# Kernel tuning notes

Measured on AMD Instinct MI355X. Metric: run time of the kernel, lower is better.

The kernel has to match this reference:

```python
import jax, jax.numpy as jnp
import numpy as np

F = 64          # n_features
H = F * F       # n_hidden = 4096
P = 4           # proj_size
T = 8192        # timesteps


def _proj_lstm_cell_zero_state(x, W_ih, W_hh, b_ih, b_hh, W_hr):
    """One PyTorch proj-LSTM layer applied per-timestep with zero initial
    (h, c). x: [T, in_dim] -> [T, P].  With h0=0, W_hh contributes 0 and
    f*c_prev vanishes."""
    h0 = jnp.zeros((x.shape[0], W_hh.shape[1]), x.dtype)
    gates = x @ W_ih.T + h0 @ W_hh.T + b_ih + b_hh          # [T, 4H]
    i, f, g, o = jnp.split(gates, 4, axis=-1)               # PyTorch gate order
    c = jax.nn.sigmoid(i) * jnp.tanh(g)                     # f*c0 = 0
    h = jax.nn.sigmoid(o) * jnp.tanh(c)                     # [T, H]
    return h @ W_hr.T                                       # [T, P]


def setup_inputs() -> dict:
    key = jax.random.key(0)
    ks = jax.random.split(key, 17)
    s = 0.05
    d = {"x": jax.random.normal(ks[0], (T, F), jnp.float32)}
    shapes = {
        "W_ih_0": (4 * H, F), "W_hh_0": (4 * H, P), "b_ih_0": (4 * H,),
        "b_hh_0": (4 * H,), "W_hr_0": (P, H),
        "W_ih_1": (4 * H, P), "W_hh_1": (4 * H, P), "b_ih_1": (4 * H,),
        "b_hh_1": (4 * H,), "W_hr_1": (P, H),
        "W_ih_2": (4 * H, P), "W_hh_2": (4 * H, P), "b_ih_2": (4 * H,),
        "b_hh_2": (4 * H,), "W_hr_2": (P, H),
    }
    for i, (name, shp) in enumerate(shapes.items()):
        d[name] = s * jax.random.normal(ks[i + 1], shp, jnp.float32)
    return d


def reference(x,
              W_ih_0, W_hh_0, b_ih_0, b_hh_0, W_hr_0,
              W_ih_1, W_hh_1, b_ih_1, b_hh_1, W_hr_1,
              W_ih_2, W_hh_2, b_ih_2, b_hh_2, W_hr_2):
    # study(): inputs.split(1, dim=0) feeds each timestep as a fresh length-1
    # sequence with zero initial state, so timesteps are independent ->
    # vectorize over T instead of the per-step Python loop.
    h = _proj_lstm_cell_zero_state(x, W_ih_0, W_hh_0, b_ih_0, b_hh_0, W_hr_0)
    h = _proj_lstm_cell_zero_state(h, W_ih_1, W_hh_1, b_ih_1, b_hh_1, W_hr_1)
    h = _proj_lstm_cell_zero_state(h, W_ih_2, W_hh_2, b_ih_2, b_hh_2, W_hr_2)
    return h  # [T, P]
```

## Files before the change

### kernel.cpp

```cpp
#include <hip/hip_runtime.h>

#define TSTEPS 8192
#define HDIM 4096
#define PDIM 4
#define KDIM 64

typedef unsigned short u16;
typedef __attribute__((ext_vector_type(8))) short short8;
typedef __attribute__((ext_vector_type(4))) float f32x4;

#define S1 -1.44269504089f
#define S2 -2.88539008177f

#if __has_builtin(__builtin_amdgcn_exp2f)
#define EXP2(x) __builtin_amdgcn_exp2f(x)
#else
#define EXP2(x) exp2f(x)
#endif
__device__ __forceinline__ float rcpf(float x) { return __builtin_amdgcn_rcpf(x); }

__device__ __forceinline__ float h_merge(float c, float ec) {
  float c2 = c * c;
  float num = c * fmaf(c2, 10.0f, 105.0f);
  float den = fmaf(c2, 45.0f, 105.0f) + c2 * c2;
  return num * rcpf(den * (1.0f + ec));
}

__device__ __forceinline__ float sig_poly(float z) {
  float z2 = z * z;
  float q = fmaf(z2, -2.1081349e-4f, 2.0833333e-3f);
  q = fmaf(z2, q, -2.0833333e-2f);
  q = fmaf(z2, q, 0.25f);
  return fmaf(z, q, 0.5f);
}
__device__ __forceinline__ float tanh_poly(float z) {
  float z2 = z * z;
  float q = fmaf(z2, -5.3968254e-2f, 1.3333333e-1f);
  q = fmaf(z2, q, -3.3333333e-1f);
  q = fmaf(z2, q, 1.0f);
  return z * q;
}

__device__ __forceinline__ void gload16(const void* g, void* l) {
  __builtin_amdgcn_global_load_lds((const __attribute__((address_space(1))) unsigned int*)g,
                                   (__attribute__((address_space(3))) unsigned int*)l,
                                   16, 0, 0);
}

__device__ __forceinline__ u16 bf16_rne(float f) {
  unsigned u = __float_as_uint(f);
  u += 0x7FFF + ((u >> 16) & 1);
  return (u16)(u >> 16);
}
__device__ __forceinline__ void hilo(float v, u16& h, u16& l) {
  h = bf16_rne(v);
  l = bf16_rne(v - __uint_as_float((unsigned)h << 16));
}

#define WS_Y0   0
#define WS_Y1   32768
#define WS_BSC  65536
#define WS_C1   77824
#define WS_C2   159744
#define WS_XHI  241664
#define WS_XLO  503808
#define WS_WHI  765952
#define WS_WLO  1159168
#define WS_PP   1552384

__global__ void prep_kernel(const float* __restrict__ x,
                            const float* __restrict__ Wih0, const float* __restrict__ bih0,
                            const float* __restrict__ bhh0,
                            const float* __restrict__ Wih1, const float* __restrict__ bih1,
                            const float* __restrict__ bhh1, const float* __restrict__ Whr1,
                            const float* __restrict__ Wih2, const float* __restrict__ bih2,
                            const float* __restrict__ bhh2, const float* __restrict__ Whr2,
                            float* __restrict__ ws) {
  const int i = blockIdx.x * 256 + threadIdx.x;
  u16* xhi = (u16*)(ws + WS_XHI);
  u16* xlo = (u16*)(ws + WS_XLO);
  u16* whi = (u16*)(ws + WS_WHI);
  u16* wlo = (u16*)(ws + WS_WLO);

  if (i < 131072) {
    float4 v = *(const float4*)&x[i * 4];
    float val[4] = {v.x, v.y, v.z, v.w};
    u16 h[4], l[4];
#pragma unroll
    for (int e = 0; e < 4; ++e) hilo(val[e], h[e], l[e]);
    *(ushort4*)&xhi[i * 4] = make_ushort4(h[0], h[1], h[2], h[3]);
    *(ushort4*)&xlo[i * 4] = make_ushort4(l[0], l[1], l[2], l[3]);
  } else if (i < 327680) {
    int f = i - 131072;
    int el4 = f * 4;
    int r = el4 >> 6;
    int k4 = el4 & 63;
    int gate = r >> 12, jr = r & 4095;
    int src = (gate == 0) ? jr : (gate + 1) * HDIM + jr;
    float sc = (gate == 1) ? S2 : S1;
    float4 v = *(const float4*)&Wih0[(size_t)src * KDIM + k4];
    float val[4] = {sc * v.x, sc * v.y, sc * v.z, sc * v.w};
    u16 h[4], l[4];
#pragma unroll
    for (int e = 0; e < 4; ++e) hilo(val[e], h[e], l[e]);
    *(ushort4*)&whi[r * KDIM + k4] = make_ushort4(h[0], h[1], h[2], h[3]);
    *(ushort4*)&wlo[r * KDIM + k4] = make_ushort4(l[0], l[1], l[2], l[3]);
  } else if (i < 339968) {
    int f = i - 327680;
    int g = f >> 12, j = f & 4095;
    int src = (g == 0) ? j : (g + 1) * HDIM + j;
    float sc = (g == 1) ? S2 : S1;
    ws[WS_BSC + f] = sc * (bih0[src] + bhh0[src]);
  } else if (i < 348160) {
    int f = i - 339968;
    const float* Wih = (f < 4096) ? Wih1 : Wih2;
    const float* bih = (f < 4096) ? bih1 : bih2;
    const float* bhh = (f < 4096) ? bhh1 : bhh2;
    const float* Whr = (f < 4096) ? Whr1 : Whr2;
    float* c = ws + ((f < 4096) ? WS_C1 : WS_C2);
    int j = f & 4095;
    float4 wi = *(const float4*)&Wih[(size_t)j * 4];
    float4 wg = *(const float4*)&Wih[(size_t)(2 * HDIM + j) * 4];
    float4 wo = *(const float4*)&Wih[(size_t)(3 * HDIM + j) * 4];
    float* cb = c + j * 20;
    *(float4*)(cb + 0)  = wi;
    *(float4*)(cb + 4)  = wg;
    *(float4*)(cb + 8)  = wo;
    *(float4*)(cb + 12) = make_float4(bih[j] + bhh[j],
                                      bih[2 * HDIM + j] + bhh[2 * HDIM + j],
                                      bih[3 * HDIM + j] + bhh[3 * HDIM + j], 0.f);
    *(float4*)(cb + 16) = make_float4(Whr[j], Whr[HDIM + j], Whr[2 * HDIM + j], Whr[3 * HDIM + j]);
  }
}

__global__ __launch_bounds__(256, 2)
void lstm_layer0_mfma(const u16* __restrict__ xhi, const u16* __restrict__ xlo,
                      const u16* __restrict__ whi, const u16* __restrict__ wlo,
                      const float* __restrict__ bsc, const float* __restrict__ Whr,
                      float* __restrict__ pp) {
  __shared__ __align__(16) char smem[65536];
  u16* lw_hi = (u16*)smem;
  u16* lw_lo = (u16*)(smem + 24576);
  u16* lx    = (u16*)(smem + 49152);

  const int tid = threadIdx.x;
  const int w = tid >> 6, lane = tid & 63;
  const int m = lane & 15, q = lane >> 4;
  const int jb = blockIdx.x & 63, tbb = blockIdx.x >> 6;
  const int j0 = jb * 64;
  const int t0 = tbb * 256;

  const int r8_ = lane >> 3;
  const int swo = ((lane & 7) ^ r8_) * 8;

#pragma unroll
  for (int ui = 0; ui < 16; ++ui) {
    const int u = w * 16 + ui;
    const u16* g;
    char* l;
    if (u < 24) {
      g = whi + (size_t)((u >> 3) * HDIM + j0 + (u & 7) * 8 + r8_) * 64 + swo;
      l = smem + u * 1024;
    } else if (u < 48) {
      int uu = u - 24;
      g = wlo + (size_t)((uu >> 3) * HDIM + j0 + (uu & 7) * 8 + r8_) * 64 + swo;
      l = smem + 24576 + uu * 1024;
    } else {
      int uu = u - 48;
      g = xhi + (size_t)(t0 + uu * 8 + r8_) * 64 + swo;
      l = smem + 49152 + uu * 1024;
    }
    gload16(g, l);
  }

  float whr_v[4][4];
#pragma unroll
  for (int p = 0; p < 4; ++p)
#pragma unroll
    for (int js = 0; js < 4; ++js)
      whr_v[p][js] = Whr[(size_t)p * HDIM + j0 + js * 16 + m];
  float biv[4], bgv[4], bov[4];
#pragma unroll
  for (int js = 0; js < 4; ++js) {
    const int j = j0 + js * 16 + m;
    biv[js] = bsc[j];
    bgv[js] = bsc[HDIM + j];
    bov[js] = bsc[2 * HDIM + j];
  }

  f32x4 acc[2][4][3];
  short8 al[2][2];

  auto zero_acc = [&]() {
#pragma unroll
    for (int ts = 0; ts < 2; ++ts)
#pragma unroll
      for (int js = 0; js < 4; ++js)
#pragma unroll
        for (int g = 0; g < 3; ++g) acc[ts][js][g] = (f32x4){0.f, 0.f, 0.f, 0.f};
  };
  auto load_al = [&](int tt) {
#pragma unroll
    for (int kc = 0; kc < 2; ++kc)
#pragma unroll
      for (int ts = 0; ts < 2; ++ts)
        al[kc][ts] = *(const short8*)&xlo[(size_t)(t0 + tt * 128 + w * 32 + ts * 16 + m) * KDIM + kc * 32 + q * 8];
  };
  auto compute = [&]() {
#pragma unroll
    for (int kc = 0; kc < 2; ++kc) {
      const int cs = ((kc * 4 + q) ^ (m & 7)) * 8;
      short8 ah[2];
#pragma unroll
      for (int ts = 0; ts < 2; ++ts)
        ah[ts] = *(const short8*)&lx[(w * 32 + ts * 16 + m) * 64 + cs];
#pragma unroll
      for (int js = 0; js < 4; ++js) {
#pragma unroll
        for (int g = 0; g < 3; ++g) {
          const int roff = (g * 64 + js * 16 + m) * 64 + cs;
          short8 bh = *(const short8*)&lw_hi[roff];
          short8 bl = *(const short8*)&lw_lo[roff];
#pragma unroll
          for (int ts = 0; ts < 2; ++ts) {
            acc[ts][js][g] = __builtin_amdgcn_mfma_f32_16x16x32_bf16(ah[ts], bh, acc[ts][js][g], 0, 0, 0);
            acc[ts][js][g] = __builtin_amdgcn_mfma_f32_16x16x32_bf16(al[kc][ts], bh, acc[ts][js][g], 0, 0, 0);
            acc[ts][js][g] = __builtin_amdgcn_mfma_f32_16x16x32_bf16(ah[ts], bl, acc[ts][js][g], 0, 0, 0);
          }
        }
      }
    }
  };
  auto act_proj = [&](int tt) {
    float hreg[2][4][4];
#pragma unroll
    for (int js = 0; js < 4; ++js) {
#pragma unroll
      for (int ts = 0; ts < 2; ++ts) {
#pragma unroll
        for (int r = 0; r < 4; ++r) {
          float ea = EXP2(acc[ts][js][0][r] + biv[js]);
          float eb = EXP2(acc[ts][js][1][r] + bgv[js]);
          float c = (1.0f - eb) * rcpf((1.0f + ea) * (1.0f + eb));
          float ec = EXP2(acc[ts][js][2][r] + bov[js]);
          hreg[ts][js][r] = h_merge(c, ec);
        }
      }
    }
#pragma unroll
    for (int ts = 0; ts < 2; ++ts) {
#pragma unroll
      for (int r = 0; r < 4; ++r) {
        float pv[4];
#pragma unroll
        for (int p = 0; p < 4; ++p) {
          float s = 0.f;
#pragma unroll
          for (int js = 0; js < 4; ++js) s = fmaf(hreg[ts][js][r], whr_v[p][js], s);
#pragma unroll
          for (int ofs = 1; ofs < 16; ofs <<= 1) s += __shfl_xor(s, ofs, 16);
          pv[p] = s;
        }
        if (m == 0) {
          const int t = t0 + tt * 128 + w * 32 + ts * 16 + q * 4 + r;
          *(float4*)&pp[((size_t)jb * TSTEPS + t) * PDIM] = make_float4(pv[0], pv[1], pv[2], pv[3]);
        }
      }
    }
  };

  load_al(0);
  zero_acc();
  __syncthreads();
  compute();
  __syncthreads();
#pragma unroll
  for (int ui = 0; ui < 4; ++ui) {
    const int u = w * 4 + ui;
    gload16(xhi + (size_t)(t0 + 128 + u * 8 + r8_) * 64 + swo, smem + 49152 + u * 1024);
  }
  load_al(1);
  act_proj(0);
  zero_acc();
  __syncthreads();
  compute();
  act_proj(1);
}

__global__ void reduce64(const float* __restrict__ pp, float* __restrict__ y) {
  const int i = blockIdx.x * 256 + threadIdx.x;
  float s = 0.f;
#pragma unroll 16
  for (int k = 0; k < 64; ++k) s += pp[(size_t)k * (TSTEPS * PDIM) + i];
  y[i] = s;
}

__global__ __launch_bounds__(256, 4)
void lstm_small(const float* __restrict__ xin, const float* __restrict__ cpk,
                float* __restrict__ pp) {
  __shared__ __align__(16) float rec[1280];
  const int tid = threadIdx.x;
  const int tc = blockIdx.x >> 6;
  const int jsp = blockIdx.x & 63;
  const int j0 = jsp * 64;

  for (int i = tid; i < 320; i += 256)
    ((float4*)rec)[i] = ((const float4*)(cpk + (size_t)j0 * 20))[i];

  const int tbase = tc * 1024 + tid;
  float4 xv[4];
#pragma unroll
  for (int s = 0; s < 4; ++s) xv[s] = ((const float4*)xin)[tbase + s * 256];
  float o[4][4];
#pragma unroll
  for (int s = 0; s < 4; ++s)
#pragma unroll
    for (int p = 0; p < 4; ++p) o[s][p] = 0.f;
  __syncthreads();

#pragma unroll 2
  for (int jj = 0; jj < 64; ++jj) {
    const float* cb = rec + jj * 20;
    float4 wi = *(const float4*)(cb + 0);
    float4 wg = *(const float4*)(cb + 4);
    float4 wo = *(const float4*)(cb + 8);
    float4 bb = *(const float4*)(cb + 12);
    float4 wr = *(const float4*)(cb + 16);
#pragma unroll
    for (int s = 0; s < 4; ++s) {
      float gi = bb.x, gg = bb.y, go = bb.z;
      gi = fmaf(xv[s].x, wi.x, gi); gi = fmaf(xv[s].y, wi.y, gi);
      gi = fmaf(xv[s].z, wi.z, gi); gi = fmaf(xv[s].w, wi.w, gi);
      gg = fmaf(xv[s].x, wg.x, gg); gg = fmaf(xv[s].y, wg.y, gg);
      gg = fmaf(xv[s].z, wg.z, gg); gg = fmaf(xv[s].w, wg.w, gg);
      go = fmaf(xv[s].x, wo.x, go); go = fmaf(xv[s].y, wo.y, go);
      go = fmaf(xv[s].z, wo.z, go); go = fmaf(xv[s].w, wo.w, go);
      float c = sig_poly(gi) * tanh_poly(gg);
      float h = tanh_poly(c) * sig_poly(go);
      o[s][0] = fmaf(h, wr.x, o[s][0]); o[s][1] = fmaf(h, wr.y, o[s][1]);
      o[s][2] = fmaf(h, wr.z, o[s][2]); o[s][3] = fmaf(h, wr.w, o[s][3]);
    }
  }

#pragma unroll
  for (int s = 0; s < 4; ++s)
    ((float4*)pp)[(size_t)jsp * TSTEPS + tbase + s * 256] =
        make_float4(o[s][0], o[s][1], o[s][2], o[s][3]);
}

extern "C" void kernel_launch(void* const* d_in, const int* in_sizes, int n_in,
                              void* d_out, int out_size, void* d_ws, size_t ws_size,
                              hipStream_t stream) {
  const float* x    = (const float*)d_in[0];
  const float* Wih0 = (const float*)d_in[1];
  const float* bih0 = (const float*)d_in[3];
  const float* bhh0 = (const float*)d_in[4];
  const float* Whr0 = (const float*)d_in[5];
  const float* Wih1 = (const float*)d_in[6];
  const float* bih1 = (const float*)d_in[8];
  const float* bhh1 = (const float*)d_in[9];
  const float* Whr1 = (const float*)d_in[10];
  const float* Wih2 = (const float*)d_in[11];
  const float* bih2 = (const float*)d_in[13];
  const float* bhh2 = (const float*)d_in[14];
  const float* Whr2 = (const float*)d_in[15];
  float* out = (float*)d_out;
  float* ws = (float*)d_ws;
  float* pp = ws + WS_PP;

  prep_kernel<<<dim3(1360), dim3(256), 0, stream>>>(
      x, Wih0, bih0, bhh0, Wih1, bih1, bhh1, Whr1, Wih2, bih2, bhh2, Whr2, ws);

  lstm_layer0_mfma<<<dim3(2048), dim3(256), 0, stream>>>(
      (const u16*)(ws + WS_XHI), (const u16*)(ws + WS_XLO),
      (const u16*)(ws + WS_WHI), (const u16*)(ws + WS_WLO),
      ws + WS_BSC, Whr0, pp);
  reduce64<<<dim3(128), dim3(256), 0, stream>>>(pp, ws + WS_Y0);

  lstm_small<<<dim3(512), dim3(256), 0, stream>>>(ws + WS_Y0, ws + WS_C1, pp);
  reduce64<<<dim3(128), dim3(256), 0, stream>>>(pp, ws + WS_Y1);

  lstm_small<<<dim3(512), dim3(256), 0, stream>>>(ws + WS_Y1, ws + WS_C2, pp);
  reduce64<<<dim3(128), dim3(256), 0, stream>>>(pp, out);
}
```

Before: 230.3 us.

## Fuse partial-sum reductions and both small LSTM layers into one kernel

```diff
diff --git a/kernel.cpp b/kernel.cpp
--- a/kernel.cpp
+++ b/kernel.cpp
@@ -119,17 +119,13 @@
     const float* Whr = (f < 4096) ? Whr1 : Whr2;
     float* c = ws + ((f < 4096) ? WS_C1 : WS_C2);
     int j = f & 4095;
-    float4 wi = *(const float4*)&Wih[(size_t)j * 4];
-    float4 wg = *(const float4*)&Wih[(size_t)(2 * HDIM + j) * 4];
-    float4 wo = *(const float4*)&Wih[(size_t)(3 * HDIM + j) * 4];
-    float* cb = c + j * 20;
-    *(float4*)(cb + 0)  = wi;
-    *(float4*)(cb + 4)  = wg;
-    *(float4*)(cb + 8)  = wo;
-    *(float4*)(cb + 12) = make_float4(bih[j] + bhh[j],
+    *(float4*)(c + j * 4)         = *(const float4*)&Wih[(size_t)j * 4];
+    *(float4*)(c + 16384 + j * 4) = *(const float4*)&Wih[(size_t)(2 * HDIM + j) * 4];
+    *(float4*)(c + 32768 + j * 4) = *(const float4*)&Wih[(size_t)(3 * HDIM + j) * 4];
+    *(float4*)(c + 49152 + j * 4) = make_float4(bih[j] + bhh[j],
                                       bih[2 * HDIM + j] + bhh[2 * HDIM + j],
                                       bih[3 * HDIM + j] + bhh[3 * HDIM + j], 0.f);
-    *(float4*)(cb + 16) = make_float4(Whr[j], Whr[HDIM + j], Whr[2 * HDIM + j], Whr[3 * HDIM + j]);
+    *(float4*)(c + 65536 + j * 4) = make_float4(Whr[j], Whr[HDIM + j], Whr[2 * HDIM + j], Whr[3 * HDIM + j]);
   }
 }
 
@@ -287,65 +283,93 @@
   act_proj(1);
 }
 
-__global__ void reduce64(const float* __restrict__ pp, float* __restrict__ y) {
-  const int i = blockIdx.x * 256 + threadIdx.x;
-  float s = 0.f;
-#pragma unroll 16
-  for (int k = 0; k < 64; ++k) s += pp[(size_t)k * (TSTEPS * PDIM) + i];
-  y[i] = s;
-}
-
-__global__ __launch_bounds__(256, 4)
-void lstm_small(const float* __restrict__ xin, const float* __restrict__ cpk,
-                float* __restrict__ pp) {
-  __shared__ __align__(16) float rec[1280];
+__global__ void fused_rest(const float* __restrict__ pp,
+                           const float* __restrict__ c1, const float* __restrict__ c2,
+                           float* __restrict__ out) {
+  __shared__ float ytile[64];
+  __shared__ float part[256];
   const int tid = threadIdx.x;
-  const int tc = blockIdx.x >> 6;
-  const int jsp = blockIdx.x & 63;
-  const int j0 = jsp * 64;
-
-  for (int i = tid; i < 320; i += 256)
-    ((float4*)rec)[i] = ((const float4*)(cpk + (size_t)j0 * 20))[i];
-
-  const int tbase = tc * 1024 + tid;
-  float4 xv[4];
-#pragma unroll
-  for (int s = 0; s < 4; ++s) xv[s] = ((const float4*)xin)[tbase + s * 256];
-  float o[4][4];
-#pragma unroll
-  for (int s = 0; s < 4; ++s)
-#pragma unroll
-    for (int p = 0; p < 4; ++p) o[s][p] = 0.f;
+  const int t0 = blockIdx.x * 16;
+  const int lane = tid & 63, w = tid >> 6;
+  const int jlane = lane & 15, tg = lane >> 4;
+
+  {
+    const int o = tid & 63;
+    const int sg = tid >> 6;
+    float s = 0.f;
+#pragma unroll 4
+    for (int k = sg * 16; k < sg * 16 + 16; ++k)
+      s += pp[(size_t)k * (TSTEPS * PDIM) + t0 * PDIM + o];
+    part[sg * 64 + o] = s;
+  }
   __syncthreads();
+  if (tid < 64) ytile[tid] = part[tid] + part[64 + tid] + part[128 + tid] + part[192 + tid];
+  __syncthreads();
+
+#pragma unroll
+  for (int L = 0; L < 2; ++L) {
+    const float* c = (L == 0) ? c1 : c2;
+    const float4* cwi = (const float4*)(c);
+    const float4* cwg = (const float4*)(c + 16384);
+    const float4* cwo = (const float4*)(c + 32768);
+    const float4* cbb = (const float4*)(c + 49152);
+    const float4* cwr = (const float4*)(c + 65536);
+
+    float4 xv[4];
+#pragma unroll
+    for (int s = 0; s < 4; ++s) xv[s] = *(const float4*)&ytile[(tg * 4 + s) * 4];
+    float o_[4][4];
+#pragma unroll
+    for (int s = 0; s < 4; ++s)
+#pragma unroll
+      for (int p = 0; p < 4; ++p) o_[s][p] = 0.f;
 
 #pragma unroll 2
-  for (int jj = 0; jj < 64; ++jj) {
-    const float* cb = rec + jj * 20;
-    float4 wi = *(const float4*)(cb + 0);
-    float4 wg = *(const float4*)(cb + 4);
-    float4 wo = *(const float4*)(cb + 8);
-    float4 bb = *(const float4*)(cb + 12);
-    float4 wr = *(const float4*)(cb + 16);
-#pragma unroll
-    for (int s = 0; s < 4; ++s) {
-      float gi = bb.x, gg = bb.y, go = bb.z;
-      gi = fmaf(xv[s].x, wi.x, gi); gi = fmaf(xv[s].y, wi.y, gi);
-      gi = fmaf(xv[s].z, wi.z, gi); gi = fmaf(xv[s].w, wi.w, gi);
-      gg = fmaf(xv[s].x, wg.x, gg); gg = fmaf(xv[s].y, wg.y, gg);
-      gg = fmaf(xv[s].z, wg.z, gg); gg = fmaf(xv[s].w, wg.w, gg);
-      go = fmaf(xv[s].x, wo.x, go); go = fmaf(xv[s].y, wo.y, go);
-      go = fmaf(xv[s].z, wo.z, go); go = fmaf(xv[s].w, wo.w, go);
-      float c = sig_poly(gi) * tanh_poly(gg);
-      float h = tanh_poly(c) * sig_poly(go);
-      o[s][0] = fmaf(h, wr.x, o[s][0]); o[s][1] = fmaf(h, wr.y, o[s][1]);
-      o[s][2] = fmaf(h, wr.z, o[s][2]); o[s][3] = fmaf(h, wr.w, o[s][3]);
-    }
-  }
-
-#pragma unroll
-  for (int s = 0; s < 4; ++s)
-    ((float4*)pp)[(size_t)jsp * TSTEPS + tbase + s * 256] =
-        make_float4(o[s][0], o[s][1], o[s][2], o[s][3]);
+    for (int jj = 0; jj < 64; ++jj) {
+      const int j = w * 1024 + jj * 16 + jlane;
+      float4 wi = cwi[j];
+      float4 wg = cwg[j];
+      float4 wo = cwo[j];
+      float4 bb = cbb[j];
+      float4 wr = cwr[j];
+#pragma unroll
+      for (int s = 0; s < 4; ++s) {
+        float gi = bb.x, gg = bb.y, go = bb.z;
+        gi = fmaf(xv[s].x, wi.x, gi); gi = fmaf(xv[s].y, wi.y, gi);
+        gi = fmaf(xv[s].z, wi.z, gi); gi = fmaf(xv[s].w, wi.w, gi);
+        gg = fmaf(xv[s].x, wg.x, gg); gg = fmaf(xv[s].y, wg.y, gg);
+        gg = fmaf(xv[s].z, wg.z, gg); gg = fmaf(xv[s].w, wg.w, gg);
+        go = fmaf(xv[s].x, wo.x, go); go = fmaf(xv[s].y, wo.y, go);
+        go = fmaf(xv[s].z, wo.z, go); go = fmaf(xv[s].w, wo.w, go);
+        float cc = sig_poly(gi) * tanh_poly(gg);
+        float h = tanh_poly(cc) * sig_poly(go);
+        o_[s][0] = fmaf(h, wr.x, o_[s][0]); o_[s][1] = fmaf(h, wr.y, o_[s][1]);
+        o_[s][2] = fmaf(h, wr.z, o_[s][2]); o_[s][3] = fmaf(h, wr.w, o_[s][3]);
+      }
+    }
+
+#pragma unroll
+    for (int s = 0; s < 4; ++s)
+#pragma unroll
+      for (int p = 0; p < 4; ++p) {
+#pragma unroll
+        for (int ofs = 1; ofs < 16; ofs <<= 1)
+          o_[s][p] += __shfl_xor(o_[s][p], ofs, 16);
+      }
+    __syncthreads();
+    if (jlane == 0) {
+#pragma unroll
+      for (int s = 0; s < 4; ++s)
+#pragma unroll
+        for (int p = 0; p < 4; ++p)
+          part[w * 64 + (tg * 4 + s) * 4 + p] = o_[s][p];
+    }
+    __syncthreads();
+    if (tid < 64) ytile[tid] = part[tid] + part[64 + tid] + part[128 + tid] + part[192 + tid];
+    __syncthreads();
+  }
+
+  if (tid < 64) out[t0 * PDIM + tid] = ytile[tid];
 }
 
 extern "C" void kernel_launch(void* const* d_in, const int* in_sizes, int n_in,
@@ -375,11 +399,6 @@
       (const u16*)(ws + WS_XHI), (const u16*)(ws + WS_XLO),
       (const u16*)(ws + WS_WHI), (const u16*)(ws + WS_WLO),
       ws + WS_BSC, Whr0, pp);
-  reduce64<<<dim3(128), dim3(256), 0, stream>>>(pp, ws + WS_Y0);
-
-  lstm_small<<<dim3(512), dim3(256), 0, stream>>>(ws + WS_Y0, ws + WS_C1, pp);
-  reduce64<<<dim3(128), dim3(256), 0, stream>>>(pp, ws + WS_Y1);
-
-  lstm_small<<<dim3(512), dim3(256), 0, stream>>>(ws + WS_Y1, ws + WS_C2, pp);
-  reduce64<<<dim3(128), dim3(256), 0, stream>>>(pp, out);
-}
+
+  fused_rest<<<dim3(512), dim3(256), 0, stream>>>(pp, ws + WS_C1, ws + WS_C2, out);
+}
```

Result: faster. 222.9 us (-3.2%).
